# Kernel optimization log

Hardware: AMD Instinct MI355X
Metric: run time of the kernel (lower is better)

The kernel has to match this reference:

```python
import jax, jax.numpy as jnp
import numpy as np

DIM = 256
HEADS = 8
DH = 32            # dim_head
CT, CH, CW = 4, 8, 8  # cuboid_size
G = 8              # global tokens
INNER = HEADS * DH
SCALE = DH ** -0.5


def setup_inputs() -> dict:
    key = jax.random.key(0)
    k0, k1, k2, k3 = jax.random.split(key, 4)
    x = jax.random.normal(k0, (2, 8, 64, 64, DIM), jnp.float32)
    Wqkv = jax.random.normal(k1, (DIM, 3 * INNER), jnp.float32) * 0.02
    Wout = jax.random.normal(k2, (INNER, DIM), jnp.float32) * 0.02
    bout = jnp.zeros((DIM,), jnp.float32)
    gtok = jax.random.normal(k3, (1, G, DIM), jnp.float32)
    return {"x": x, "Wqkv": Wqkv, "Wout": Wout, "bout": bout, "gtok": gtok}


def reference(x, Wqkv, Wout, bout, gtok):
    b, t, h, w, d = x.shape
    pad_t = (-t) % CT
    pad_h = (-h) % CH
    pad_w = (-w) % CW
    # F.pad(..., mode='replicate') on trailing spatial dims == edge padding
    xp = jnp.pad(x, ((0, 0), (0, pad_t), (0, pad_h), (0, pad_w), (0, 0)), mode="edge")
    nt, nh, nw = xp.shape[1], xp.shape[2], xp.shape[3]
    Tn, Hn, Wn = nt // CT, nh // CH, nw // CW
    # partition into cuboid windows: (b*Tn*Hn*Wn, CT*CH*CW, d)
    xc = xp.reshape(b, Tn, CT, Hn, CH, Wn, CW, d)
    xc = xc.transpose(0, 1, 3, 5, 2, 4, 6, 7).reshape(b * Tn * Hn * Wn, CT * CH * CW, d)
    nB = xc.shape[0]
    # prepend shared global tokens
    g = jnp.broadcast_to(gtok, (nB, G, d))
    xc = jnp.concatenate([g, xc], axis=1)  # (nB, G + cuboid_len, d)
    # qkv projection and head split
    qkv = xc @ Wqkv
    q, k, v = jnp.split(qkv, 3, axis=-1)

    def to_heads(z):  # (nB, n, INNER) -> (nB, HEADS, n, DH)
        return z.reshape(nB, z.shape[1], HEADS, DH).transpose(0, 2, 1, 3)

    q, k, v = to_heads(q), to_heads(k), to_heads(v)
    attn = jax.nn.softmax(jnp.einsum("bhid,bhjd->bhij", q, k) * SCALE, axis=-1)
    o = jnp.einsum("bhij,bhjd->bhid", attn, v)
    o = o.transpose(0, 2, 1, 3).reshape(nB, -1, INNER)
    o = o @ Wout + bout
    o = o[:, G:, :]  # drop global tokens
    # un-partition back to (b, nt, nh, nw, d)
    o = o.reshape(b, Tn, Hn, Wn, CT, CH, CW, d)
    o = o.transpose(0, 1, 4, 2, 5, 3, 6, 7).reshape(b, nt, nh, nw, d)
    return o[:, :t, :h, :w, :]
```

## Files before the change

### kernel.cpp

```cpp
#include <hip/hip_runtime.h>
#include <math.h>

typedef short short8 __attribute__((ext_vector_type(8)));
typedef float f32x4 __attribute__((ext_vector_type(4)));

static constexpr float SCALE = 0.17677669529663687f;

__device__ __forceinline__ ushort f2bf(float x) {
    uint u = __float_as_uint(x);
    u += 0x7fff + ((u >> 16) & 1);
    return (ushort)(u >> 16);
}

__device__ __forceinline__ const float* row_src(
    int bb, int tok, const float* __restrict__ x, const float* __restrict__ gt)
{
    if (tok < 8) return gt + tok * 256;
    int j = tok - 8;
    int wn = bb & 7, hn = (bb >> 3) & 7, tn = (bb >> 6) & 1, b = bb >> 7;
    int cw = j & 7, ch = (j >> 3) & 7, ct = j >> 6;
    return x + ((((size_t)(b * 8 + tn * 4 + ct)) * 64 + (hn * 8 + ch)) * 64
                + (wn * 8 + cw)) * 256;
}

union F8 { ushort4 q[2]; short8 v; };

__global__ __launch_bounds__(256)
void k_prep(const float* __restrict__ Wq, const float* __restrict__ Wo,
            ushort* __restrict__ WqtH, ushort* __restrict__ WotH)
{
    int i = blockIdx.x * 256 + threadIdx.x;
    if (i < 196608) {
        uint k = (uint)i / 768u, n = (uint)i - k * 768u;
        WqtH[n * 256 + k] = f2bf(Wq[i]);
    } else {
        int j = i - 196608;
        uint k = (uint)j >> 8, n = (uint)j & 255u;
        WotH[n * 256 + k] = f2bf(Wo[j]);
    }
}

#define GP 36
__global__ __launch_bounds__(256, 4)
void k_qkv(const float* __restrict__ x, const ushort* __restrict__ WtH,
           const float* __restrict__ gt, ushort* __restrict__ qkv,
           int nb, int bb0, int mrows)
{
    int g = blockIdx.x;
    int xcd = g & 7;
    int j6 = g >> 3;
    int m_t = (j6 / 6) * 8 + xcd;
    int n_t = j6 % 6;
    if (m_t >= nb) return;
    const int m0 = m_t * 128, n0 = n_t * 128;

    __shared__ ushort SM[2 * 128 * GP];
    ushort* Ah = SM;
    ushort* Bh = SM + 128 * GP;
    const int tid = threadIdx.x;
    const int lane = tid & 63, wid = tid >> 6;
    const int ln = lane & 15, lg = lane >> 4;
    const int wm = wid >> 1, wn = wid & 1;

    const int srow = tid >> 1;
    const int kh = (tid & 1) * 16;
    int mst = m0 + srow;
    if (mst >= mrows) mst = mrows - 1;
    int lb = mst / 264, tok = mst - lb * 264;
    const float* rsrc = row_src(bb0 + lb, tok, x, gt);
    const ushort* bsrcH = WtH + (size_t)(n0 + srow) * 256 + kh;

    f32x4 acc[4][4];
#pragma unroll
    for (int i = 0; i < 4; ++i)
#pragma unroll
        for (int j = 0; j < 4; ++j) acc[i][j] = (f32x4){0.f, 0.f, 0.f, 0.f};

    float4 apre[4];
    ushort4 bpre[4];
#pragma unroll
    for (int j = 0; j < 4; ++j) {
        apre[j] = *(const float4*)(rsrc + kh + 4 * j);
        bpre[j] = *(const ushort4*)(bsrcH + 4 * j);
    }

    for (int kt = 0; kt < 256; kt += 32) {
        __syncthreads();
#pragma unroll
        for (int j = 0; j < 4; ++j) {
            *(ushort4*)&Ah[srow * GP + kh + 4 * j] =
                make_ushort4(f2bf(apre[j].x), f2bf(apre[j].y), f2bf(apre[j].z), f2bf(apre[j].w));
            *(ushort4*)&Bh[srow * GP + kh + 4 * j] = bpre[j];
        }
        __syncthreads();

        if (kt + 32 < 256) {
#pragma unroll
            for (int j = 0; j < 4; ++j) {
                apre[j] = *(const float4*)(rsrc + kt + 32 + kh + 4 * j);
                bpre[j] = *(const ushort4*)(bsrcH + kt + 32 + 4 * j);
            }
        }

        short8 af[4], bf[4];
#pragma unroll
        for (int mi = 0; mi < 4; ++mi) {
            int base = (wm * 64 + mi * 16 + ln) * GP + 4 * lg;
            F8 t;
            t.q[0] = *(const ushort4*)&Ah[base]; t.q[1] = *(const ushort4*)&Ah[base + 16];
            af[mi] = t.v;
        }
#pragma unroll
        for (int ni = 0; ni < 4; ++ni) {
            int base = (wn * 64 + ni * 16 + ln) * GP + 4 * lg;
            F8 t;
            t.q[0] = *(const ushort4*)&Bh[base]; t.q[1] = *(const ushort4*)&Bh[base + 16];
            bf[ni] = t.v;
        }
#pragma unroll
        for (int mi = 0; mi < 4; ++mi)
#pragma unroll
            for (int ni = 0; ni < 4; ++ni)
                acc[mi][ni] = __builtin_amdgcn_mfma_f32_16x16x32_bf16(af[mi], bf[ni], acc[mi][ni], 0, 0, 0);
    }

    float* Tr = (float*)SM;
    const int trow = tid >> 3;
    const int t8 = (tid & 7) * 8;
#pragma unroll
    for (int mi = 0; mi < 4; ++mi) {
        __syncthreads();
#pragma unroll
        for (int ni = 0; ni < 4; ++ni)
#pragma unroll
            for (int r = 0; r < 4; ++r)
                Tr[(wm * 16 + lg * 4 + r) * 132 + wn * 64 + ni * 16 + ln] = acc[mi][ni][r];
        __syncthreads();
        int gm = m0 + (trow >> 4) * 64 + mi * 16 + (trow & 15);
        if (gm < mrows) {
            ushort* dst = qkv + (size_t)gm * 768 + n0;
            const float* src = &Tr[trow * 132];
#pragma unroll
            for (int half = 0; half < 2; ++half) {
                float4 a = *(const float4*)(src + half * 64 + t8);
                float4 b = *(const float4*)(src + half * 64 + t8 + 4);
                union { ushort4 u4[2]; int4 i4; } pk;
                pk.u4[0] = make_ushort4(f2bf(a.x), f2bf(a.y), f2bf(a.z), f2bf(a.w));
                pk.u4[1] = make_ushort4(f2bf(b.x), f2bf(b.y), f2bf(b.z), f2bf(b.w));
                *(int4*)(dst + half * 64 + t8) = pk.i4;
            }
        }
    }
}

#define KPAD 36
#define VPAD 296
__global__ __launch_bounds__(256, 4)
void k_attn(ushort* __restrict__ qkv)
{
    __shared__ ushort Khi[272 * KPAD];
    __shared__ ushort Vt[32 * VPAD];

    const int lb = blockIdx.x, h = blockIdx.y;
    const int tid = threadIdx.x;
    const int wid = tid >> 6;
    const int lane = tid & 63;
    const int ln = lane & 15, lg = lane >> 4;
    ushort* base = qkv + (size_t)lb * (264 * 768);
    const int koff = 256 + h * 32, voff = 512 + h * 32;

    for (int slot = tid; slot < 1056; slot += 256) {
        int rp = slot >> 3;
        int c4 = (slot & 7) * 4;
        int r0 = rp * 2;
        const ushort* p0 = base + (size_t)r0 * 768;
        const ushort* p1 = p0 + 768;
        ushort4 k0 = *(const ushort4*)(p0 + koff + c4);
        ushort4 k1 = *(const ushort4*)(p1 + koff + c4);
        ushort4 v0 = *(const ushort4*)(p0 + voff + c4);
        ushort4 v1 = *(const ushort4*)(p1 + voff + c4);
        *(ushort4*)&Khi[r0 * KPAD + c4] = k0;
        *(ushort4*)&Khi[(r0 + 1) * KPAD + c4] = k1;
        *(ushort2*)&Vt[(c4 + 0) * VPAD + r0] = make_ushort2(v0.x, v1.x);
        *(ushort2*)&Vt[(c4 + 1) * VPAD + r0] = make_ushort2(v0.y, v1.y);
        *(ushort2*)&Vt[(c4 + 2) * VPAD + r0] = make_ushort2(v0.z, v1.z);
        *(ushort2*)&Vt[(c4 + 3) * VPAD + r0] = make_ushort2(v0.w, v1.w);
    }
    for (int slot = tid; slot < 1024; slot += 256) {
        int d = slot >> 5;
        Vt[d * VPAD + 264 + (slot & 31)] = 0;
    }

    short8 qh[4];
#pragma unroll
    for (int t = 0; t < 4; ++t) {
        int qrow = 8 + (wid * 4 + t) * 16 + ln;
        const ushort* qp = base + (size_t)qrow * 768 + h * 32;
        F8 fh;
        fh.q[0] = *(const ushort4*)(qp + 4 * lg);
        fh.q[1] = *(const ushort4*)(qp + 16 + 4 * lg);
        qh[t] = fh.v;
    }

    f32x4 acc[4][2];
    float lsum[4];
#pragma unroll
    for (int t = 0; t < 4; ++t) {
        acc[t][0] = (f32x4){0.f, 0.f, 0.f, 0.f};
        acc[t][1] = (f32x4){0.f, 0.f, 0.f, 0.f};
        lsum[t] = 0.f;
    }

    __syncthreads();

    for (int g = 0; g < 8; ++g) {
        const int kt0 = g * 32;
        F8 fa;
        const ushort* pka = &Khi[(kt0 + ln) * KPAD + 4 * lg];
        fa.q[0] = *(const ushort4*)pka; fa.q[1] = *(const ushort4*)(pka + 16);
        short8 ka = fa.v;
        const ushort* pkb = &Khi[(kt0 + 16 + ln) * KPAD + 4 * lg];
        fa.q[0] = *(const ushort4*)pkb; fa.q[1] = *(const ushort4*)(pkb + 16);
        short8 kb = fa.v;
        const ushort* pv0 = &Vt[ln * VPAD + kt0 + 4 * lg];
        fa.q[0] = *(const ushort4*)pv0; fa.q[1] = *(const ushort4*)(pv0 + 16);
        short8 va = fa.v;
        const ushort* pv1 = &Vt[(16 + ln) * VPAD + kt0 + 4 * lg];
        fa.q[0] = *(const ushort4*)pv1; fa.q[1] = *(const ushort4*)(pv1 + 16);
        short8 vb = fa.v;

#pragma unroll
        for (int t = 0; t < 4; ++t) {
            f32x4 sa = {0.f, 0.f, 0.f, 0.f}, sb = {0.f, 0.f, 0.f, 0.f};
            sa = __builtin_amdgcn_mfma_f32_16x16x32_bf16(ka, qh[t], sa, 0, 0, 0);
            sb = __builtin_amdgcn_mfma_f32_16x16x32_bf16(kb, qh[t], sb, 0, 0, 0);
            float p[8];
#pragma unroll
            for (int c = 0; c < 4; ++c) {
                p[c] = __expf(sa[c] * SCALE);
                p[4 + c] = __expf(sb[c] * SCALE);
            }
            lsum[t] += ((p[0] + p[1]) + (p[2] + p[3])) + ((p[4] + p[5]) + (p[6] + p[7]));
            F8 pf;
            pf.q[0] = make_ushort4(f2bf(p[0]), f2bf(p[1]), f2bf(p[2]), f2bf(p[3]));
            pf.q[1] = make_ushort4(f2bf(p[4]), f2bf(p[5]), f2bf(p[6]), f2bf(p[7]));
            acc[t][0] = __builtin_amdgcn_mfma_f32_16x16x32_bf16(va, pf.v, acc[t][0], 0, 0, 0);
            acc[t][1] = __builtin_amdgcn_mfma_f32_16x16x32_bf16(vb, pf.v, acc[t][1], 0, 0, 0);
        }
    }

    {
        F8 fa;
        const ushort* pka = &Khi[(256 + ln) * KPAD + 4 * lg];
        fa.q[0] = *(const ushort4*)pka; fa.q[1] = *(const ushort4*)(pka + 16);
        short8 ka = fa.v;
        const ushort* pv0 = &Vt[ln * VPAD + 256 + 4 * lg];
        fa.q[0] = *(const ushort4*)pv0; fa.q[1] = *(const ushort4*)(pv0 + 16);
        short8 va = fa.v;
        const ushort* pv1 = &Vt[(16 + ln) * VPAD + 256 + 4 * lg];
        fa.q[0] = *(const ushort4*)pv1; fa.q[1] = *(const ushort4*)(pv1 + 16);
        short8 vb = fa.v;

#pragma unroll
        for (int t = 0; t < 4; ++t) {
            f32x4 sa = {0.f, 0.f, 0.f, 0.f};
            sa = __builtin_amdgcn_mfma_f32_16x16x32_bf16(ka, qh[t], sa, 0, 0, 0);
            float p[4];
#pragma unroll
            for (int c = 0; c < 4; ++c)
                p[c] = (lg >= 2) ? 0.f : __expf(sa[c] * SCALE);
            lsum[t] += (p[0] + p[1]) + (p[2] + p[3]);
            F8 pf;
            pf.q[0] = make_ushort4(f2bf(p[0]), f2bf(p[1]), f2bf(p[2]), f2bf(p[3]));
            pf.q[1] = make_ushort4(0, 0, 0, 0);
            acc[t][0] = __builtin_amdgcn_mfma_f32_16x16x32_bf16(va, pf.v, acc[t][0], 0, 0, 0);
            acc[t][1] = __builtin_amdgcn_mfma_f32_16x16x32_bf16(vb, pf.v, acc[t][1], 0, 0, 0);
        }
    }

#pragma unroll
    for (int t = 0; t < 4; ++t) {
        float l = lsum[t];
        l += __shfl_xor(l, 16);
        l += __shfl_xor(l, 32);
        float inv = 1.f / l;
        ushort* op = base + (size_t)(8 + (wid * 4 + t) * 16 + ln) * 768 + h * 32;
#pragma unroll
        for (int r = 0; r < 4; ++r) {
            op[lg * 4 + r] = f2bf(acc[t][0][r] * inv);
            op[16 + lg * 4 + r] = f2bf(acc[t][1][r] * inv);
        }
    }
}

__global__ __launch_bounds__(256, 4)
void k_out(const ushort* __restrict__ qkv, const ushort* __restrict__ WtH,
           const float* __restrict__ bias, float* __restrict__ out, int bb0)
{
    __shared__ ushort SM[2 * 128 * GP];
    ushort* Ah = SM;
    ushort* Bh = SM + 128 * GP;
    const int tid = threadIdx.x;
    const int lane = tid & 63, wid = tid >> 6;
    const int ln = lane & 15, lg = lane >> 4;
    const int wm = wid >> 1, wn = wid & 1;
    const int n0 = blockIdx.x * 128, m0 = blockIdx.y * 128;

    const int srow = tid >> 1;
    const int kh = (tid & 1) * 16;
    int mst = m0 + srow;
    int lb = mst >> 8, j0 = mst & 255;
    const ushort* rsrc = qkv + (size_t)(lb * 264 + 8 + j0) * 768;
    const ushort* bsrcH = WtH + (size_t)(n0 + srow) * 256 + kh;

    f32x4 acc[4][4];
#pragma unroll
    for (int i = 0; i < 4; ++i)
#pragma unroll
        for (int j = 0; j < 4; ++j) acc[i][j] = (f32x4){0.f, 0.f, 0.f, 0.f};

    ushort4 apre[4], bpre[4];
#pragma unroll
    for (int j = 0; j < 4; ++j) {
        apre[j] = *(const ushort4*)(rsrc + kh + 4 * j);
        bpre[j] = *(const ushort4*)(bsrcH + 4 * j);
    }

    for (int kt = 0; kt < 256; kt += 32) {
        __syncthreads();
#pragma unroll
        for (int j = 0; j < 4; ++j) {
            *(ushort4*)&Ah[srow * GP + kh + 4 * j] = apre[j];
            *(ushort4*)&Bh[srow * GP + kh + 4 * j] = bpre[j];
        }
        __syncthreads();

        if (kt + 32 < 256) {
#pragma unroll
            for (int j = 0; j < 4; ++j) {
                apre[j] = *(const ushort4*)(rsrc + kt + 32 + kh + 4 * j);
                bpre[j] = *(const ushort4*)(bsrcH + kt + 32 + 4 * j);
            }
        }

        short8 af[4], bf[4];
#pragma unroll
        for (int mi = 0; mi < 4; ++mi) {
            int base = (wm * 64 + mi * 16 + ln) * GP + 4 * lg;
            F8 t;
            t.q[0] = *(const ushort4*)&Ah[base]; t.q[1] = *(const ushort4*)&Ah[base + 16];
            af[mi] = t.v;
        }
#pragma unroll
        for (int ni = 0; ni < 4; ++ni) {
            int base = (wn * 64 + ni * 16 + ln) * GP + 4 * lg;
            F8 t;
            t.q[0] = *(const ushort4*)&Bh[base]; t.q[1] = *(const ushort4*)&Bh[base + 16];
            bf[ni] = t.v;
        }
#pragma unroll
        for (int mi = 0; mi < 4; ++mi)
#pragma unroll
            for (int ni = 0; ni < 4; ++ni)
                acc[mi][ni] = __builtin_amdgcn_mfma_f32_16x16x32_bf16(af[mi], bf[ni], acc[mi][ni], 0, 0, 0);
    }

    float bcol[4];
#pragma unroll
    for (int ni = 0; ni < 4; ++ni) bcol[ni] = bias[n0 + wn * 64 + ni * 16 + ln];

    float* Tr = (float*)SM;
    const int trow = tid >> 3;
    const int tc = (tid & 7) * 4;
#pragma unroll
    for (int mi = 0; mi < 4; ++mi) {
        __syncthreads();
#pragma unroll
        for (int ni = 0; ni < 4; ++ni)
#pragma unroll
            for (int r = 0; r < 4; ++r)
                Tr[(wm * 16 + lg * 4 + r) * 132 + wn * 64 + ni * 16 + ln] = acc[mi][ni][r] + bcol[ni];
        __syncthreads();
        int m = m0 + (trow >> 4) * 64 + mi * 16 + (trow & 15);
        int lb2 = m >> 8, j = m & 255;
        int bb = bb0 + lb2;
        int wn2 = bb & 7, hn = (bb >> 3) & 7, tn = (bb >> 6) & 1, b = bb >> 7;
        int cw = j & 7, ch = (j >> 3) & 7, ct = j >> 6;
        float* dst = out + ((((size_t)(b * 8 + tn * 4 + ct)) * 64 + (hn * 8 + ch)) * 64
                            + (wn2 * 8 + cw)) * 256 + n0;
        const float* src = &Tr[trow * 132];
#pragma unroll
        for (int jj = 0; jj < 4; ++jj)
            *(float4*)(dst + tc + 32 * jj) = *(const float4*)(src + tc + 32 * jj);
    }
}

extern "C" void kernel_launch(void* const* d_in, const int* in_sizes, int n_in,
                              void* d_out, int out_size, void* d_ws, size_t ws_size,
                              hipStream_t stream) {
    const float* x    = (const float*)d_in[0];
    const float* Wqkv = (const float*)d_in[1];
    const float* Wout = (const float*)d_in[2];
    const float* bout = (const float*)d_in[3];
    const float* gtok = (const float*)d_in[4];
    float* out = (float*)d_out;

    ushort* WqtH = (ushort*)d_ws;
    ushort* WotH = WqtH + 196608;
    ushort* qkv = (ushort*)((char*)d_ws + 1048576);

    k_prep<<<1024, 256, 0, stream>>>(Wqkv, Wout, WqtH, WotH);

    const size_t per_block = (size_t)264 * 768 * 2;
    int P = (int)((ws_size - 1048576) / per_block);
    if (P > 256) P = 256;
    if (P < 1) P = 1;

    for (int bb0 = 0; bb0 < 256; bb0 += P) {
        int pb = (256 - bb0 < P) ? (256 - bb0) : P;
        int mrows = pb * 264;
        int nb = (mrows + 127) / 128;
        int grid1 = 8 * (((nb + 7) / 8) * 6);
        k_qkv<<<dim3(grid1), 256, 0, stream>>>(x, WqtH, gtok, qkv, nb, bb0, mrows);
        k_attn<<<dim3(pb, 8), 256, 0, stream>>>(qkv);
        k_out<<<dim3(2, pb * 2), 256, 0, stream>>>(qkv, WotH, bout, out, bb0);
    }
}
```

Measured before the change: 135.9 us.

## Pre-gather cuboid rows to bf16 buffer and double-buffer GEMM register prefetch

Adds a gather kernel that reads the windowed x rows (plus global tokens) once, converts them to bf16 and writes them into a contiguous buffer. The QKV GEMM then loads bf16 rows directly instead of fp32 with in-loop conversion, which avoids reading each x row six times (once per N tile) as fp32. Both GEMMs now prefetch two K-steps ahead using a two-set register ring with a fully unrolled loop. The cost is an extra kernel launch, an extra global write and read of the gathered buffer, higher register use, and less workspace left for the qkv chunk.

```diff
diff --git a/kernel.cpp b/kernel.cpp
--- a/kernel.cpp
+++ b/kernel.cpp
@@ -40,11 +40,27 @@
     }
 }
 
+__global__ __launch_bounds__(256)
+void k_gath(const float* __restrict__ x, const float* __restrict__ gt,
+            ushort* __restrict__ xg)
+{
+    int idx = blockIdx.x * 256 + threadIdx.x;
+    int row = idx >> 5;
+    int c = (idx & 31) * 8;
+    int bb = row / 264, tok = row - bb * 264;
+    const float* src = row_src(bb, tok, x, gt) + c;
+    float4 a = *(const float4*)src;
+    float4 b = *(const float4*)(src + 4);
+    union { ushort4 u4[2]; int4 i4; } pk;
+    pk.u4[0] = make_ushort4(f2bf(a.x), f2bf(a.y), f2bf(a.z), f2bf(a.w));
+    pk.u4[1] = make_ushort4(f2bf(b.x), f2bf(b.y), f2bf(b.z), f2bf(b.w));
+    *(int4*)(xg + (size_t)row * 256 + c) = pk.i4;
+}
+
 #define GP 36
 __global__ __launch_bounds__(256, 4)
-void k_qkv(const float* __restrict__ x, const ushort* __restrict__ WtH,
-           const float* __restrict__ gt, ushort* __restrict__ qkv,
-           int nb, int bb0, int mrows)
+void k_qkv(const ushort* __restrict__ xg, const ushort* __restrict__ WtH,
+           ushort* __restrict__ qkv, int nb, int bb0, int mrows)
 {
     int g = blockIdx.x;
     int xcd = g & 7;
@@ -66,8 +82,7 @@
     const int kh = (tid & 1) * 16;
     int mst = m0 + srow;
     if (mst >= mrows) mst = mrows - 1;
-    int lb = mst / 264, tok = mst - lb * 264;
-    const float* rsrc = row_src(bb0 + lb, tok, x, gt);
+    const ushort* rsrc = xg + (size_t)mst * 256 + kh;
     const ushort* bsrcH = WtH + (size_t)(n0 + srow) * 256 + kh;
 
     f32x4 acc[4][4];
@@ -76,29 +91,32 @@
 #pragma unroll
         for (int j = 0; j < 4; ++j) acc[i][j] = (f32x4){0.f, 0.f, 0.f, 0.f};
 
-    float4 apre[4];
-    ushort4 bpre[4];
+    ushort4 aset[2][4], bset[2][4];
 #pragma unroll
     for (int j = 0; j < 4; ++j) {
-        apre[j] = *(const float4*)(rsrc + kh + 4 * j);
-        bpre[j] = *(const ushort4*)(bsrcH + 4 * j);
-    }
-
-    for (int kt = 0; kt < 256; kt += 32) {
+        aset[0][j] = *(const ushort4*)(rsrc + 4 * j);
+        bset[0][j] = *(const ushort4*)(bsrcH + 4 * j);
+        aset[1][j] = *(const ushort4*)(rsrc + 32 + 4 * j);
+        bset[1][j] = *(const ushort4*)(bsrcH + 32 + 4 * j);
+    }
+
+#pragma unroll
+    for (int it = 0; it < 8; ++it) {
+        const int s = it & 1;
         __syncthreads();
 #pragma unroll
         for (int j = 0; j < 4; ++j) {
-            *(ushort4*)&Ah[srow * GP + kh + 4 * j] =
-                make_ushort4(f2bf(apre[j].x), f2bf(apre[j].y), f2bf(apre[j].z), f2bf(apre[j].w));
-            *(ushort4*)&Bh[srow * GP + kh + 4 * j] = bpre[j];
-        }
-        __syncthreads();
-
-        if (kt + 32 < 256) {
+            *(ushort4*)&Ah[srow * GP + kh + 4 * j] = aset[s][j];
+            *(ushort4*)&Bh[srow * GP + kh + 4 * j] = bset[s][j];
+        }
+        __syncthreads();
+
+        if (it + 2 < 8) {
+            const int ktn = 32 * (it + 2);
 #pragma unroll
             for (int j = 0; j < 4; ++j) {
-                apre[j] = *(const float4*)(rsrc + kt + 32 + kh + 4 * j);
-                bpre[j] = *(const ushort4*)(bsrcH + kt + 32 + 4 * j);
+                aset[s][j] = *(const ushort4*)(rsrc + ktn + 4 * j);
+                bset[s][j] = *(const ushort4*)(bsrcH + ktn + 4 * j);
             }
         }
 
@@ -319,27 +337,32 @@
 #pragma unroll
         for (int j = 0; j < 4; ++j) acc[i][j] = (f32x4){0.f, 0.f, 0.f, 0.f};
 
-    ushort4 apre[4], bpre[4];
+    ushort4 aset[2][4], bset[2][4];
 #pragma unroll
     for (int j = 0; j < 4; ++j) {
-        apre[j] = *(const ushort4*)(rsrc + kh + 4 * j);
-        bpre[j] = *(const ushort4*)(bsrcH + 4 * j);
-    }
-
-    for (int kt = 0; kt < 256; kt += 32) {
+        aset[0][j] = *(const ushort4*)(rsrc + kh + 4 * j);
+        bset[0][j] = *(const ushort4*)(bsrcH + 4 * j);
+        aset[1][j] = *(const ushort4*)(rsrc + kh + 32 + 4 * j);
+        bset[1][j] = *(const ushort4*)(bsrcH + 32 + 4 * j);
+    }
+
+#pragma unroll
+    for (int it = 0; it < 8; ++it) {
+        const int s = it & 1;
         __syncthreads();
 #pragma unroll
         for (int j = 0; j < 4; ++j) {
-            *(ushort4*)&Ah[srow * GP + kh + 4 * j] = apre[j];
-            *(ushort4*)&Bh[srow * GP + kh + 4 * j] = bpre[j];
-        }
-        __syncthreads();
-
-        if (kt + 32 < 256) {
+            *(ushort4*)&Ah[srow * GP + kh + 4 * j] = aset[s][j];
+            *(ushort4*)&Bh[srow * GP + kh + 4 * j] = bset[s][j];
+        }
+        __syncthreads();
+
+        if (it + 2 < 8) {
+            const int ktn = 32 * (it + 2);
 #pragma unroll
             for (int j = 0; j < 4; ++j) {
-                apre[j] = *(const ushort4*)(rsrc + kt + 32 + kh + 4 * j);
-                bpre[j] = *(const ushort4*)(bsrcH + kt + 32 + 4 * j);
+                aset[s][j] = *(const ushort4*)(rsrc + kh + ktn + 4 * j);
+                bset[s][j] = *(const ushort4*)(bsrcH + ktn + 4 * j);
             }
         }
 
@@ -407,12 +430,15 @@
 
     ushort* WqtH = (ushort*)d_ws;
     ushort* WotH = WqtH + 196608;
-    ushort* qkv = (ushort*)((char*)d_ws + 1048576);
+    ushort* xg   = (ushort*)((char*)d_ws + 1048576);
+    ushort* qkv  = xg + (size_t)67584 * 256;
 
     k_prep<<<1024, 256, 0, stream>>>(Wqkv, Wout, WqtH, WotH);
-
+    k_gath<<<8448, 256, 0, stream>>>(x, gtok, xg);
+
+    const size_t head = 1048576 + (size_t)67584 * 256 * 2;
     const size_t per_block = (size_t)264 * 768 * 2;
-    int P = (int)((ws_size - 1048576) / per_block);
+    int P = (int)((ws_size - head) / per_block);
     if (P > 256) P = 256;
     if (P < 1) P = 1;
 
@@ -421,7 +447,7 @@
         int mrows = pb * 264;
         int nb = (mrows + 127) / 128;
         int grid1 = 8 * (((nb + 7) / 8) * 6);
-        k_qkv<<<dim3(grid1), 256, 0, stream>>>(x, WqtH, gtok, qkv, nb, bb0, mrows);
+        k_qkv<<<dim3(grid1), 256, 0, stream>>>(xg + (size_t)bb0 * 264 * 256, WqtH, qkv, nb, bb0, mrows);
         k_attn<<<dim3(pb, 8), 256, 0, stream>>>(qkv);
         k_out<<<dim3(2, pb * 2), 256, 0, stream>>>(qkv, WotH, bout, out, bb0);
     }
```

New measurement: 145.7 us. 1.07x slower.
